# Kernel optimization log

Measured on AMD Instinct MI355X. Metric: run time of the kernel, lower is better.

The kernel has to match this reference:

```python
import jax, jax.numpy as jnp
import numpy as np

LN_EPS = 1e-5
IH_IDX = np.array([0, 2, 4, 6])  # layernorm_iih, fih, aih, oih
HH_IDX = np.array([1, 3, 5, 7])  # layernorm_ihh, fhh, ahh, ohh


def _ln(x, g, b):
    # LayerNorm over last dim, matching nn.LayerNorm(hidden_size)
    mu = jnp.mean(x, axis=-1, keepdims=True)
    xc = x - mu
    var = jnp.mean(xc * xc, axis=-1, keepdims=True)
    return g * xc * jax.lax.rsqrt(var + LN_EPS) + b


def setup_inputs() -> dict:
    B, I, H = 4096, 1024, 1024
    key = jax.random.key(0)
    ks = jax.random.split(key, 8)
    stdv = 1.0 / np.sqrt(H)  # reset_parameters: uniform(-stdv, stdv)
    return {
        "x": jax.random.normal(ks[0], (B, I), jnp.float32),
        "h": jax.random.normal(ks[1], (B, H), jnp.float32),
        "c": jax.random.normal(ks[2], (B, H), jnp.float32),
        "w_ih": jax.random.uniform(ks[3], (4 * H, I), jnp.float32, -stdv, stdv),
        "w_hh": jax.random.uniform(ks[4], (4 * H, H), jnp.float32, -stdv, stdv),
        "b_ih": jax.random.uniform(ks[5], (4 * H,), jnp.float32, -stdv, stdv),
        # 9 LayerNorms stacked: [iih, ihh, fih, fhh, aih, ahh, oih, ohh, ct]
        "ln_gamma": 1.0 + 0.1 * jax.random.normal(ks[6], (9, H), jnp.float32),
        "ln_beta": 0.1 * jax.random.normal(ks[7], (9, H), jnp.float32),
        "time": 0,
    }


def reference(x, h, c, w_ih, w_hh, b_ih, ln_gamma, ln_beta, time):
    B = x.shape[0]
    H = w_hh.shape[1]
    # pre-activations, split into the 4 gates (i, f, a, o) along dim 1
    pre_ih = (x @ w_ih.T).reshape(B, 4, H)   # [B,4,H]
    pre_hh = (h @ w_hh.T).reshape(B, 4, H)   # [B,4,H]
    # per-gate LayerNorm on ih and hh contributions, then add bias
    gates = (
        _ln(pre_ih, ln_gamma[IH_IDX], ln_beta[IH_IDX])
        + _ln(pre_hh, ln_gamma[HH_IDX], ln_beta[HH_IDX])
        + b_ih.reshape(4, H)
    )
    i, f, a, o = gates[:, 0], gates[:, 1], gates[:, 2], gates[:, 3]
    c_new = jax.nn.sigmoid(f) * c + jax.nn.sigmoid(i) * jnp.tanh(a)
    h_new = jax.nn.sigmoid(o) * jnp.tanh(_ln(c_new, ln_gamma[8], ln_beta[8]))
    return (h_new, c_new)
```

## Files before the change

kernel.cpp:

```cpp
#include <hip/hip_runtime.h>
#include <hip/hip_bf16.h>
#include <stdint.h>


#define HDIM 1024
#define BATCH 4096
#define NGATE 4096
#define KDIM 1024

typedef __bf16 bf16x8 __attribute__((ext_vector_type(8)));
typedef float f32x4 __attribute__((ext_vector_type(4)));

__device__ __forceinline__ unsigned short f2bf(float f) {
  unsigned int u = __builtin_bit_cast(unsigned int, f);
  unsigned int r = (u + 0x7fffu + ((u >> 16) & 1u)) >> 16;
  return (unsigned short)r;
}

__device__ __forceinline__ float bf2f(unsigned short s) {
  unsigned int u = ((unsigned int)s) << 16;
  return __builtin_bit_cast(float, u);
}

__device__ __forceinline__ void gl_lds16(const void* g, void* l) {
  __builtin_amdgcn_global_load_lds(
      (__attribute__((address_space(1))) unsigned int*)g,
      (__attribute__((address_space(3))) unsigned int*)l,
      16, 0, 0);
}

__global__ __launch_bounds__(256) void cast_bf16_kernel(
    const float* __restrict__ x, const float* __restrict__ h,
    const float* __restrict__ wi, const float* __restrict__ wh,
    unsigned short* __restrict__ xb, unsigned short* __restrict__ hb,
    unsigned short* __restrict__ wib, unsigned short* __restrict__ whb) {
  const float* src;
  unsigned short* dst;
  switch (blockIdx.y) {
    case 0: src = x;  dst = xb;  break;
    case 1: src = h;  dst = hb;  break;
    case 2: src = wi; dst = wib; break;
    default: src = wh; dst = whb; break;
  }
  size_t i = ((size_t)blockIdx.x * 256 + threadIdx.x) * 4;
  float4 v = *(const float4*)(src + i);
  ushort4 o;
  o.x = f2bf(v.x); o.y = f2bf(v.y); o.z = f2bf(v.z); o.w = f2bf(v.w);
  *(ushort4*)(dst + i) = o;
}

__global__ __launch_bounds__(256, 2) void gemm_bt_kernel(
    const unsigned short* __restrict__ A0, const unsigned short* __restrict__ B0,
    unsigned short* __restrict__ C0,
    const unsigned short* __restrict__ A1, const unsigned short* __restrict__ B1,
    unsigned short* __restrict__ C1) {
  const unsigned short* A = blockIdx.z ? A1 : A0;
  const unsigned short* B = blockIdx.z ? B1 : B0;
  unsigned short* C = blockIdx.z ? C1 : C0;

  __shared__ alignas(16) unsigned short As[128 * 32];
  __shared__ alignas(16) unsigned short Bs[128 * 32];

  const int tid = threadIdx.x;
  const int wave = tid >> 6;
  const int lane = tid & 63;
  const int bm = blockIdx.x * 128;
  const int bn = blockIdx.y * 128;
  const int wm = (wave >> 1) * 64;
  const int wn = (wave & 1) * 64;

  const int srow = lane >> 2;
  const int scol = (lane & 3) * 8;

  f32x4 acc[4][4];
#pragma unroll
  for (int i = 0; i < 4; ++i)
#pragma unroll
    for (int j = 0; j < 4; ++j)
#pragma unroll
      for (int r = 0; r < 4; ++r) acc[i][j][r] = 0.0f;

  const int m15 = lane & 15;
  const int quad = lane >> 4;

  for (int k0 = 0; k0 < KDIM; k0 += 32) {
#pragma unroll
    for (int t = 0; t < 2; ++t) {
      int chunk = wave * 32 + t * 16;
      int row = chunk + srow;
      gl_lds16(A + (size_t)(bm + row) * KDIM + k0 + scol, &As[chunk * 32]);
      gl_lds16(B + (size_t)(bn + row) * KDIM + k0 + scol, &Bs[chunk * 32]);
    }
    __syncthreads();

    bf16x8 af[4], bfr[4];
#pragma unroll
    for (int i = 0; i < 4; ++i)
      af[i] = *(const bf16x8*)&As[(wm + i * 16 + m15) * 32 + quad * 8];
#pragma unroll
    for (int j = 0; j < 4; ++j)
      bfr[j] = *(const bf16x8*)&Bs[(wn + j * 16 + m15) * 32 + quad * 8];

#pragma unroll
    for (int i = 0; i < 4; ++i)
#pragma unroll
      for (int j = 0; j < 4; ++j)
        acc[i][j] = __builtin_amdgcn_mfma_f32_16x16x32_bf16(af[i], bfr[j], acc[i][j], 0, 0, 0);

    __syncthreads();
  }

#pragma unroll
  for (int i = 0; i < 4; ++i)
#pragma unroll
    for (int j = 0; j < 4; ++j)
#pragma unroll
      for (int r = 0; r < 4; ++r) {
        int m = bm + wm + i * 16 + quad * 4 + r;
        int n = bn + wn + j * 16 + m15;
        C[(size_t)m * NGATE + n] = f2bf(acc[i][j][r]);
      }
}

__device__ __forceinline__ void block_sum4(float v[4], float* lds, int tid) {
#pragma unroll
  for (int o = 32; o > 0; o >>= 1)
#pragma unroll
    for (int k = 0; k < 4; ++k) v[k] += __shfl_down(v[k], o, 64);
  __syncthreads();
  if ((tid & 63) == 0) {
    int w = tid >> 6;
#pragma unroll
    for (int k = 0; k < 4; ++k) lds[w * 4 + k] = v[k];
  }
  __syncthreads();
#pragma unroll
  for (int k = 0; k < 4; ++k) v[k] = lds[k] + lds[4 + k] + lds[8 + k] + lds[12 + k];
}

__device__ __forceinline__ float sigmoidf_(float x) {
  return 1.0f / (1.0f + __expf(-x));
}

__global__ __launch_bounds__(256) void ln_gate_kernel(
    const unsigned short* __restrict__ pih, const unsigned short* __restrict__ phh,
    const float* __restrict__ c, const float* __restrict__ b_ih,
    const float* __restrict__ gamma, const float* __restrict__ beta,
    float* __restrict__ h_out, float* __restrict__ c_out) {
  __shared__ float lds[16];
  const int b = blockIdx.x;
  const int t = threadIdx.x;
  const float inv_h = 1.0f / 1024.0f;
  const float eps = 1e-5f;

  float gate[4][4];

#pragma unroll
  for (int g = 0; g < 4; ++g) {
    float vih[4], vhh[4];
    float red[4] = {0.f, 0.f, 0.f, 0.f};
#pragma unroll
    for (int r = 0; r < 4; ++r) {
      int j = t + 256 * r;
      float a = bf2f(pih[(size_t)b * NGATE + g * HDIM + j]);
      float e = bf2f(phh[(size_t)b * NGATE + g * HDIM + j]);
      vih[r] = a; vhh[r] = e;
      red[0] += a; red[1] += a * a; red[2] += e; red[3] += e * e;
    }
    block_sum4(red, lds, t);
    float mu0 = red[0] * inv_h;
    float rs0 = rsqrtf(red[1] * inv_h - mu0 * mu0 + eps);
    float mu1 = red[2] * inv_h;
    float rs1 = rsqrtf(red[3] * inv_h - mu1 * mu1 + eps);
#pragma unroll
    for (int r = 0; r < 4; ++r) {
      int j = t + 256 * r;
      float gih = gamma[(2 * g) * HDIM + j] * ((vih[r] - mu0) * rs0) + beta[(2 * g) * HDIM + j];
      float ghh = gamma[(2 * g + 1) * HDIM + j] * ((vhh[r] - mu1) * rs1) + beta[(2 * g + 1) * HDIM + j];
      gate[g][r] = gih + ghh + b_ih[g * HDIM + j];
    }
  }

  float cn[4], ov[4];
  float red2[4] = {0.f, 0.f, 0.f, 0.f};
#pragma unroll
  for (int r = 0; r < 4; ++r) {
    int j = t + 256 * r;
    float iv = sigmoidf_(gate[0][r]);
    float fv = sigmoidf_(gate[1][r]);
    float av = tanhf(gate[2][r]);
    ov[r] = sigmoidf_(gate[3][r]);
    float cv = fv * c[(size_t)b * HDIM + j] + iv * av;
    cn[r] = cv;
    red2[0] += cv; red2[1] += cv * cv;
  }
  block_sum4(red2, lds, t);
  float mu = red2[0] * inv_h;
  float rs = rsqrtf(red2[1] * inv_h - mu * mu + eps);
#pragma unroll
  for (int r = 0; r < 4; ++r) {
    int j = t + 256 * r;
    float ln = gamma[8 * HDIM + j] * ((cn[r] - mu) * rs) + beta[8 * HDIM + j];
    h_out[(size_t)b * HDIM + j] = ov[r] * tanhf(ln);
    c_out[(size_t)b * HDIM + j] = cn[r];
  }
}

extern "C" void kernel_launch(void* const* d_in, const int* in_sizes, int n_in,
                              void* d_out, int out_size, void* d_ws, size_t ws_size,
                              hipStream_t stream) {
  const float* x     = (const float*)d_in[0];
  const float* h     = (const float*)d_in[1];
  const float* c     = (const float*)d_in[2];
  const float* w_ih  = (const float*)d_in[3];
  const float* w_hh  = (const float*)d_in[4];
  const float* b_ih  = (const float*)d_in[5];
  const float* gamma = (const float*)d_in[6];
  const float* beta  = (const float*)d_in[7];

  char* ws = (char*)d_ws;
  unsigned short* xb  = (unsigned short*)(ws);
  unsigned short* hb  = (unsigned short*)(ws + (size_t)8 * 1024 * 1024);
  unsigned short* wib = (unsigned short*)(ws + (size_t)16 * 1024 * 1024);
  unsigned short* whb = (unsigned short*)(ws + (size_t)24 * 1024 * 1024);
  unsigned short* pih = (unsigned short*)(ws + (size_t)32 * 1024 * 1024);
  unsigned short* phh = (unsigned short*)(ws + (size_t)64 * 1024 * 1024);

  dim3 cgrid(4096, 4, 1);
  cast_bf16_kernel<<<cgrid, 256, 0, stream>>>(x, h, w_ih, w_hh, xb, hb, wib, whb);

  dim3 ggrid(32, 32, 2);
  gemm_bt_kernel<<<ggrid, 256, 0, stream>>>(xb, wib, pih, hb, whb, phh);

  float* h_out = (float*)d_out;
  float* c_out = h_out + (size_t)BATCH * HDIM;
  ln_gate_kernel<<<4096, 256, 0, stream>>>(pih, phh, c, b_ih, gamma, beta, h_out, c_out);
}
```

Baseline: 257.7 us.

## Swizzle GEMM LDS tiles and vectorize LN-gate epilogue with fast transcendentals

The GEMM's LDS staging now XOR-swizzles the 16-byte column chunk per row, with a matching swizzle on the fragment reads, to cut LDS bank conflicts on the MFMA operand loads. The LN/gate kernel now has each thread own four contiguous elements, so inputs, parameters and outputs move as vector loads and stores. It also swaps tanhf and the sigmoid division for exp plus hardware reciprocal, which trades a little accuracy for fewer instructions. The GEMM, the dominant cost, is only touched by the swizzle.

```diff
diff --git a/kernel.cpp b/kernel.cpp
--- a/kernel.cpp
+++ b/kernel.cpp
@@ -70,7 +70,7 @@
   const int wn = (wave & 1) * 64;
 
   const int srow = lane >> 2;
-  const int scol = (lane & 3) * 8;
+  const int scol = (((lane & 3) ^ ((lane >> 3) & 3)) * 8);
 
   f32x4 acc[4][4];
 #pragma unroll
@@ -82,6 +82,7 @@
 
   const int m15 = lane & 15;
   const int quad = lane >> 4;
+  const int rdoff = ((quad ^ ((m15 >> 1) & 3)) * 8);
 
   for (int k0 = 0; k0 < KDIM; k0 += 32) {
 #pragma unroll
@@ -96,10 +97,10 @@
     bf16x8 af[4], bfr[4];
 #pragma unroll
     for (int i = 0; i < 4; ++i)
-      af[i] = *(const bf16x8*)&As[(wm + i * 16 + m15) * 32 + quad * 8];
+      af[i] = *(const bf16x8*)&As[(wm + i * 16 + m15) * 32 + rdoff];
 #pragma unroll
     for (int j = 0; j < 4; ++j)
-      bfr[j] = *(const bf16x8*)&Bs[(wn + j * 16 + m15) * 32 + quad * 8];
+      bfr[j] = *(const bf16x8*)&Bs[(wn + j * 16 + m15) * 32 + rdoff];
 
 #pragma unroll
     for (int i = 0; i < 4; ++i)
@@ -138,8 +139,11 @@
   for (int k = 0; k < 4; ++k) v[k] = lds[k] + lds[4 + k] + lds[8 + k] + lds[12 + k];
 }
 
-__device__ __forceinline__ float sigmoidf_(float x) {
-  return 1.0f / (1.0f + __expf(-x));
+__device__ __forceinline__ float fast_sigmoid(float x) {
+  return __builtin_amdgcn_rcpf(1.0f + __expf(-x));
+}
+__device__ __forceinline__ float fast_tanh(float x) {
+  return 1.0f - 2.0f * __builtin_amdgcn_rcpf(__expf(2.0f * x) + 1.0f);
 }
 
 __global__ __launch_bounds__(256) void ln_gate_kernel(
@@ -150,6 +154,7 @@
   __shared__ float lds[16];
   const int b = blockIdx.x;
   const int t = threadIdx.x;
+  const int j = t * 4;
   const float inv_h = 1.0f / 1024.0f;
   const float eps = 1e-5f;
 
@@ -157,53 +162,68 @@
 
 #pragma unroll
   for (int g = 0; g < 4; ++g) {
-    float vih[4], vhh[4];
+    ushort4 a4 = *(const ushort4*)&pih[(size_t)b * NGATE + g * HDIM + j];
+    ushort4 e4 = *(const ushort4*)&phh[(size_t)b * NGATE + g * HDIM + j];
+    float vih[4] = {bf2f(a4.x), bf2f(a4.y), bf2f(a4.z), bf2f(a4.w)};
+    float vhh[4] = {bf2f(e4.x), bf2f(e4.y), bf2f(e4.z), bf2f(e4.w)};
     float red[4] = {0.f, 0.f, 0.f, 0.f};
 #pragma unroll
     for (int r = 0; r < 4; ++r) {
-      int j = t + 256 * r;
-      float a = bf2f(pih[(size_t)b * NGATE + g * HDIM + j]);
-      float e = bf2f(phh[(size_t)b * NGATE + g * HDIM + j]);
-      vih[r] = a; vhh[r] = e;
-      red[0] += a; red[1] += a * a; red[2] += e; red[3] += e * e;
+      red[0] += vih[r]; red[1] += vih[r] * vih[r];
+      red[2] += vhh[r]; red[3] += vhh[r] * vhh[r];
     }
     block_sum4(red, lds, t);
     float mu0 = red[0] * inv_h;
     float rs0 = rsqrtf(red[1] * inv_h - mu0 * mu0 + eps);
     float mu1 = red[2] * inv_h;
     float rs1 = rsqrtf(red[3] * inv_h - mu1 * mu1 + eps);
+    float4 g0 = *(const float4*)&gamma[(2 * g) * HDIM + j];
+    float4 b0 = *(const float4*)&beta[(2 * g) * HDIM + j];
+    float4 g1 = *(const float4*)&gamma[(2 * g + 1) * HDIM + j];
+    float4 b1 = *(const float4*)&beta[(2 * g + 1) * HDIM + j];
+    float4 bb = *(const float4*)&b_ih[g * HDIM + j];
+    const float* g0p = &g0.x; const float* b0p = &b0.x;
+    const float* g1p = &g1.x; const float* b1p = &b1.x;
+    const float* bbp = &bb.x;
 #pragma unroll
     for (int r = 0; r < 4; ++r) {
-      int j = t + 256 * r;
-      float gih = gamma[(2 * g) * HDIM + j] * ((vih[r] - mu0) * rs0) + beta[(2 * g) * HDIM + j];
-      float ghh = gamma[(2 * g + 1) * HDIM + j] * ((vhh[r] - mu1) * rs1) + beta[(2 * g + 1) * HDIM + j];
-      gate[g][r] = gih + ghh + b_ih[g * HDIM + j];
+      float gih = g0p[r] * ((vih[r] - mu0) * rs0) + b0p[r];
+      float ghh = g1p[r] * ((vhh[r] - mu1) * rs1) + b1p[r];
+      gate[g][r] = gih + ghh + bbp[r];
     }
   }
 
+  float4 cv4 = *(const float4*)&c[(size_t)b * HDIM + j];
+  const float* cvp = &cv4.x;
   float cn[4], ov[4];
   float red2[4] = {0.f, 0.f, 0.f, 0.f};
 #pragma unroll
   for (int r = 0; r < 4; ++r) {
-    int j = t + 256 * r;
-    float iv = sigmoidf_(gate[0][r]);
-    float fv = sigmoidf_(gate[1][r]);
-    float av = tanhf(gate[2][r]);
-    ov[r] = sigmoidf_(gate[3][r]);
-    float cv = fv * c[(size_t)b * HDIM + j] + iv * av;
-    cn[r] = cv;
-    red2[0] += cv; red2[1] += cv * cv;
+    float iv = fast_sigmoid(gate[0][r]);
+    float fv = fast_sigmoid(gate[1][r]);
+    float av = fast_tanh(gate[2][r]);
+    ov[r] = fast_sigmoid(gate[3][r]);
+    float cvn = fv * cvp[r] + iv * av;
+    cn[r] = cvn;
+    red2[0] += cvn; red2[1] += cvn * cvn;
   }
   block_sum4(red2, lds, t);
   float mu = red2[0] * inv_h;
   float rs = rsqrtf(red2[1] * inv_h - mu * mu + eps);
+
+  float4 g8 = *(const float4*)&gamma[8 * HDIM + j];
+  float4 b8 = *(const float4*)&beta[8 * HDIM + j];
+  const float* g8p = &g8.x; const float* b8p = &b8.x;
+  float4 ho, co;
+  float* hop = &ho.x; float* cop = &co.x;
 #pragma unroll
   for (int r = 0; r < 4; ++r) {
-    int j = t + 256 * r;
-    float ln = gamma[8 * HDIM + j] * ((cn[r] - mu) * rs) + beta[8 * HDIM + j];
-    h_out[(size_t)b * HDIM + j] = ov[r] * tanhf(ln);
-    c_out[(size_t)b * HDIM + j] = cn[r];
-  }
+    float ln = g8p[r] * ((cn[r] - mu) * rs) + b8p[r];
+    hop[r] = ov[r] * fast_tanh(ln);
+    cop[r] = cn[r];
+  }
+  *(float4*)&h_out[(size_t)b * HDIM + j] = ho;
+  *(float4*)&c_out[(size_t)b * HDIM + j] = co;
 }
 
 extern "C" void kernel_launch(void* const* d_in, const int* in_sizes, int n_in,
```

New measurement: 250.8 us. -2.7%, faster.
